# Kernel tuning notes

Hardware: AMD Instinct MI355X
Metric: run time of the kernel (lower is better)

## Reference

```python
import jax, jax.numpy as jnp
import numpy as np

L, N, C = 128, 32, 128
DIM_MLP, OUT = 128, 128


def setup_inputs() -> dict:
    key = jax.random.key(0)
    ks = jax.random.split(key, 6)
    s_in2 = 1.0 / np.sqrt(2 * C)
    s_mid = 1.0 / np.sqrt(DIM_MLP)
    s_in = 1.0 / np.sqrt(C)
    return {
        "x": jax.random.normal(ks[0], (L, N, C), jnp.float32),
        "attn_w1": jax.random.normal(ks[1], (2 * C, DIM_MLP), jnp.float32) * s_in2,
        "attn_b1": jnp.zeros((DIM_MLP,), jnp.float32),
        "attn_w2": jax.random.normal(ks[2], (DIM_MLP, OUT), jnp.float32) * s_mid,
        "attn_b2": jnp.zeros((OUT,), jnp.float32),
        "value_w1": jax.random.normal(ks[3], (C, DIM_MLP), jnp.float32) * s_in,
        "value_b1": jnp.zeros((DIM_MLP,), jnp.float32),
        "value_w2": jax.random.normal(ks[4], (DIM_MLP, OUT), jnp.float32) * s_mid,
        "value_b2": jnp.zeros((OUT,), jnp.float32),
    }


def reference(x, attn_w1, attn_b1, attn_w2, attn_b2,
              value_w1, value_b1, value_w2, value_b2):
    l, n, c = x.shape
    # Outer concat: pair[i, j, b] = concat(x[i, b], x[j, b])  -> (l, l, N, 2C)
    xi = jnp.broadcast_to(x[:, None, :, :], (l, l, n, c))
    xj = jnp.broadcast_to(x[None, :, :, :], (l, l, n, c))
    pair = jnp.concatenate([xi, xj], axis=-1)
    # Pairwise attention MLP (ReLU hidden, linear output)
    h = jax.nn.relu(pair @ attn_w1 + attn_b1)          # (l, l, N, dim_mlp)
    attn = h @ attn_w2 + attn_b2                       # (l, l, N, out)
    # Value MLP
    hv = jax.nn.relu(x @ value_w1 + value_b1)          # (l, N, dim_mlp)
    value = hv @ value_w2 + value_b2                   # (l, N, out)
    # Elementwise weighted reduce over key axis j (NOT a matmul over channels)
    out = jnp.einsum('ijbc,jbc->ibc', attn, value)     # (l, N, out)
    return out
```

## Files before the change

kernel.cpp:

```cpp
#include <hip/hip_runtime.h>
#include <hip/hip_bf16.h>

#define L_DIM 128
#define N_DIM 32
#define C_DIM 128
#define K_DIM 128
#define OUT_DIM 128

#define Q_STRIDE  132
#define VT_STRIDE 20

typedef __attribute__((ext_vector_type(8))) short short8;
typedef __attribute__((ext_vector_type(4))) float float4v;

static __device__ __forceinline__ short bf16_bits(float f) {
    __bf16 h = (__bf16)f;
    return __builtin_bit_cast(short, h);
}

__global__ __launch_bounds__(256) void k_pre(
    const float* __restrict__ x,
    const float* __restrict__ attn_w1, const float* __restrict__ attn_b1,
    const float* __restrict__ attn_w2,
    const float* __restrict__ value_w1, const float* __restrict__ value_b1,
    const float* __restrict__ value_w2, const float* __restrict__ value_b2,
    float* __restrict__ P, float* __restrict__ Q, float* __restrict__ Vt,
    short* __restrict__ W2s)
{
    int bid = blockIdx.x;
    if (bid >= 512) {
        int e = (bid - 512) * 256 + threadIdx.x;
        int idx  = e & 7;
        int colr = (e >> 3) & 15;
        int quad = (e >> 7) & 3;
        int mi   = (e >> 9) & 3;
        int ct   = e >> 11;
        int k = quad * 8 + 32 * mi + idx;
        int c = ct * 16 + colr;
        W2s[e] = bf16_bits(attn_w2[k * OUT_DIM + c]);
        return;
    }

    __shared__ float xs[8][C_DIM];
    __shared__ float hvs[8][K_DIM];
    int tid = threadIdx.x;
    int b   = bid >> 4;
    int i0g = (bid & 15) * 8;

    {
        int f = tid * 4;
        int row = f >> 7, c = f & 127;
        *(float4v*)(&xs[row][c]) =
            *(const float4v*)(x + ((size_t)(i0g + row) * N_DIM + b) * C_DIM + c);
    }
    __syncthreads();

    int ks   = tid & 127;
    int half = tid >> 7;

    float pacc[4] = {0,0,0,0};
    float qacc[4] = {0,0,0,0};
    float hacc[4] = {0,0,0,0};
    #pragma unroll 4
    for (int c = 0; c < C_DIM; ++c) {
        float wa = attn_w1[c * K_DIM + ks];
        float wb = attn_w1[(C_DIM + c) * K_DIM + ks];
        float wv = value_w1[c * K_DIM + ks];
        #pragma unroll
        for (int r = 0; r < 4; ++r) {
            float xr = xs[half * 4 + r][c];
            pacc[r] = fmaf(xr, wa, pacc[r]);
            qacc[r] = fmaf(xr, wb, qacc[r]);
            hacc[r] = fmaf(xr, wv, hacc[r]);
        }
    }
    float b1 = attn_b1[ks], vb1 = value_b1[ks];
    #pragma unroll
    for (int r = 0; r < 4; ++r) {
        int i = i0g + half * 4 + r;
        P[((size_t)b * L_DIM + i) * K_DIM + ks] = pacc[r];
        Q[((size_t)b * L_DIM + i) * K_DIM + ks] = qacc[r] + b1;
        hvs[half * 4 + r][ks] = fmaxf(hacc[r] + vb1, 0.f);
    }
    __syncthreads();

    float vacc[4] = {0,0,0,0};
    #pragma unroll 4
    for (int k = 0; k < K_DIM; ++k) {
        float w = value_w2[k * OUT_DIM + ks];
        #pragma unroll
        for (int r = 0; r < 4; ++r)
            vacc[r] = fmaf(hvs[half * 4 + r][k], w, vacc[r]);
    }
    float vb2 = value_b2[ks];
    float4v vout = { vacc[0] + vb2, vacc[1] + vb2, vacc[2] + vb2, vacc[3] + vb2 };
    *(float4v*)(Vt + ((size_t)b * OUT_DIM + ks) * L_DIM + i0g + half * 4) = vout;
}

__global__ __launch_bounds__(256, 2)
void k_main(
    const float* __restrict__ P, const float* __restrict__ Q,
    const float* __restrict__ Vt,
    const short* __restrict__ W2s, const float* __restrict__ attn_b2,
    float* __restrict__ out)
{
    __shared__ float Q_lds[2][16 * Q_STRIDE];
    __shared__ float Vt_lds[2][128 * VT_STRIDE];

    int b    = blockIdx.x >> 5;
    int it4  = blockIdx.x & 31;
    int tid  = threadIdx.x;
    int wave = tid >> 6;
    int lane = tid & 63;
    int quad = lane >> 4;
    int col  = lane & 15;
    int ip   = wave >> 1;
    int cth  = wave & 1;
    int i0   = it4 * 4 + ip * 2;

    short8 bfrag[4][4];
    const short8* w2p = (const short8*)W2s;
    #pragma unroll
    for (int cl = 0; cl < 4; ++cl)
        #pragma unroll
        for (int mi = 0; mi < 4; ++mi)
            bfrag[cl][mi] =
                w2p[(((cth * 4 + cl) * 4 + mi) * 4 + quad) * 16 + col];

    float4v pf[2][4][2];
    #pragma unroll
    for (int ii = 0; ii < 2; ++ii) {
        const float* Pp = P + ((size_t)b * L_DIM + i0 + ii) * K_DIM + quad * 8;
        #pragma unroll
        for (int ksl = 0; ksl < 4; ++ksl) {
            pf[ii][ksl][0] = *(const float4v*)(Pp + ksl * 32);
            pf[ii][ksl][1] = *(const float4v*)(Pp + ksl * 32 + 4);
        }
    }

    int srow = tid >> 4;
    int sc8  = (tid & 15) * 8;
    int cs   = tid >> 1;
    int ch   = (tid & 1) * 8;
    const float* Qbase = Q  + (size_t)b * L_DIM * K_DIM;
    const float* Vbase = Vt + (size_t)b * OUT_DIM * L_DIM;

    {
        const float* qp = Qbase + srow * K_DIM + sc8;
        float4v qa = *(const float4v*)qp, qb = *(const float4v*)(qp + 4);
        *(float4v*)&Q_lds[0][srow * Q_STRIDE + sc8]     = qa;
        *(float4v*)&Q_lds[0][srow * Q_STRIDE + sc8 + 4] = qb;
        const float* vp = Vbase + cs * L_DIM + ch;
        float4v va = *(const float4v*)vp, vb = *(const float4v*)(vp + 4);
        *(float4v*)&Vt_lds[0][cs * VT_STRIDE + ch]     = va;
        *(float4v*)&Vt_lds[0][cs * VT_STRIDE + ch + 4] = vb;
    }
    __syncthreads();

    float acc0[4] = {0.f, 0.f, 0.f, 0.f};
    float acc1[4] = {0.f, 0.f, 0.f, 0.f};
    float sv[4]   = {0.f, 0.f, 0.f, 0.f};

    for (int r = 0; r < 8; ++r) {
        int cur = r & 1;

        float4v nqa, nqb, nva, nvb;
        if (r < 7) {
            const float* qp = Qbase + ((r + 1) * 16 + srow) * K_DIM + sc8;
            nqa = *(const float4v*)qp; nqb = *(const float4v*)(qp + 4);
            const float* vp = Vbase + cs * L_DIM + (r + 1) * 16 + ch;
            nva = *(const float4v*)vp; nvb = *(const float4v*)(vp + 4);
        }

        short8 af[2][4];
        const float* Qc = &Q_lds[cur][col * Q_STRIDE + quad * 8];
        #pragma unroll
        for (int ksl = 0; ksl < 4; ++ksl) {
            float4v q0 = *(const float4v*)(Qc + ksl * 32);
            float4v q1 = *(const float4v*)(Qc + ksl * 32 + 4);
            #pragma unroll
            for (int ii = 0; ii < 2; ++ii) {
                float4v s0 = pf[ii][ksl][0] + q0;
                float4v s1 = pf[ii][ksl][1] + q1;
                short8 a;
                #pragma unroll
                for (int t = 0; t < 4; ++t) {
                    a[t]     = bf16_bits(fmaxf(s0[t], 0.f));
                    a[t + 4] = bf16_bits(fmaxf(s1[t], 0.f));
                }
                af[ii][ksl] = a;
            }
        }

        const float* Vc = &Vt_lds[cur][0];
        #pragma unroll
        for (int cl = 0; cl < 4; ++cl) {
            float4v c40 = {0.f, 0.f, 0.f, 0.f};
            float4v c41 = {0.f, 0.f, 0.f, 0.f};
            #pragma unroll
            for (int ksl = 0; ksl < 4; ++ksl) {
                c40 = __builtin_amdgcn_mfma_f32_16x16x32_bf16(
                        af[0][ksl], bfrag[cl][ksl], c40, 0, 0, 0);
                c41 = __builtin_amdgcn_mfma_f32_16x16x32_bf16(
                        af[1][ksl], bfrag[cl][ksl], c41, 0, 0, 0);
            }
            int cc = cth * 64 + cl * 16 + col;
            float4v vv = *(const float4v*)(Vc + cc * VT_STRIDE + quad * 4);
            #pragma unroll
            for (int rr = 0; rr < 4; ++rr) {
                acc0[cl] = fmaf(c40[rr], vv[rr], acc0[cl]);
                acc1[cl] = fmaf(c41[rr], vv[rr], acc1[cl]);
                sv[cl]  += vv[rr];
            }
        }

        if (r < 7) {
            int nxt = cur ^ 1;
            *(float4v*)&Q_lds[nxt][srow * Q_STRIDE + sc8]      = nqa;
            *(float4v*)&Q_lds[nxt][srow * Q_STRIDE + sc8 + 4]  = nqb;
            *(float4v*)&Vt_lds[nxt][cs * VT_STRIDE + ch]       = nva;
            *(float4v*)&Vt_lds[nxt][cs * VT_STRIDE + ch + 4]   = nvb;
            __syncthreads();
        }
    }

    #pragma unroll
    for (int cl = 0; cl < 4; ++cl) {
        acc0[cl] += __shfl_xor(acc0[cl], 16, 64);
        acc0[cl] += __shfl_xor(acc0[cl], 32, 64);
        acc1[cl] += __shfl_xor(acc1[cl], 16, 64);
        acc1[cl] += __shfl_xor(acc1[cl], 32, 64);
        sv[cl]   += __shfl_xor(sv[cl], 16, 64);
        sv[cl]   += __shfl_xor(sv[cl], 32, 64);
    }

    if (quad == 0) {
        #pragma unroll
        for (int cl = 0; cl < 4; ++cl) {
            int cc = cth * 64 + cl * 16 + col;
            float bsv = attn_b2[cc] * sv[cl];
            out[((size_t)i0 * N_DIM + b) * OUT_DIM + cc]       = acc0[cl] + bsv;
            out[((size_t)(i0 + 1) * N_DIM + b) * OUT_DIM + cc] = acc1[cl] + bsv;
        }
    }
}

extern "C" void kernel_launch(void* const* d_in, const int* in_sizes, int n_in,
                              void* d_out, int out_size, void* d_ws, size_t ws_size,
                              hipStream_t stream)
{
    const float* x        = (const float*)d_in[0];
    const float* attn_w1  = (const float*)d_in[1];
    const float* attn_b1  = (const float*)d_in[2];
    const float* attn_w2  = (const float*)d_in[3];
    const float* attn_b2  = (const float*)d_in[4];
    const float* value_w1 = (const float*)d_in[5];
    const float* value_b1 = (const float*)d_in[6];
    const float* value_w2 = (const float*)d_in[7];
    const float* value_b2 = (const float*)d_in[8];
    float* out = (float*)d_out;

    float* ws  = (float*)d_ws;
    float* P   = ws;
    float* Q   = ws + 524288;
    float* Vt  = ws + 1048576;
    short* W2s = (short*)(ws + 1572864);

    k_pre<<<576, 256, 0, stream>>>(x, attn_w1, attn_b1, attn_w2,
                                   value_w1, value_b1, value_w2, value_b2,
                                   P, Q, Vt, W2s);
    k_main<<<1024, 256, 0, stream>>>(P, Q, Vt, W2s, attn_b2, out);
}
```

Baseline: 126.1 us.

## Stage Q/V/P tiles via direct global-to-LDS loads with XOR swizzle

```diff
diff --git a/kernel.cpp b/kernel.cpp
--- a/kernel.cpp
+++ b/kernel.cpp
@@ -7,15 +7,18 @@
 #define K_DIM 128
 #define OUT_DIM 128
 
-#define Q_STRIDE  132
-#define VT_STRIDE 20
-
 typedef __attribute__((ext_vector_type(8))) short short8;
 typedef __attribute__((ext_vector_type(4))) float float4v;
 
 static __device__ __forceinline__ short bf16_bits(float f) {
     __bf16 h = (__bf16)f;
     return __builtin_bit_cast(short, h);
+}
+
+static __device__ __forceinline__ void gl_lds16(const float* g, float* l) {
+    __builtin_amdgcn_global_load_lds(
+        (const __attribute__((address_space(1))) unsigned int*)g,
+        (__attribute__((address_space(3))) unsigned int*)l, 16, 0, 0);
 }
 
 __global__ __launch_bounds__(256) void k_pre(
@@ -97,15 +100,17 @@
     *(float4v*)(Vt + ((size_t)b * OUT_DIM + ks) * L_DIM + i0g + half * 4) = vout;
 }
 
-__global__ __launch_bounds__(256, 2)
+__global__ __launch_bounds__(256)
+__attribute__((amdgpu_waves_per_eu(3)))
 void k_main(
     const float* __restrict__ P, const float* __restrict__ Q,
     const float* __restrict__ Vt,
     const short* __restrict__ W2s, const float* __restrict__ attn_b2,
     float* __restrict__ out)
 {
-    __shared__ float Q_lds[2][16 * Q_STRIDE];
-    __shared__ float Vt_lds[2][128 * VT_STRIDE];
+    __shared__ float Q_lds[2][16 * 128];
+    __shared__ float V_lds[2][128 * 16];
+    __shared__ float P_lds[4 * 128];
 
     int b    = blockIdx.x >> 5;
     int it4  = blockIdx.x & 31;
@@ -116,7 +121,9 @@
     int col  = lane & 15;
     int ip   = wave >> 1;
     int cth  = wave & 1;
-    int i0   = it4 * 4 + ip * 2;
+
+    const float* Qbase = Q  + (size_t)b * L_DIM * K_DIM;
+    const float* Vbase = Vt + (size_t)b * OUT_DIM * L_DIM;
 
     short8 bfrag[4][4];
     const short8* w2p = (const short8*)W2s;
@@ -127,61 +134,69 @@
             bfrag[cl][mi] =
                 w2p[(((cth * 4 + cl) * 4 + mi) * 4 + quad) * 16 + col];
 
-    float4v pf[2][4][2];
-    #pragma unroll
-    for (int ii = 0; ii < 2; ++ii) {
-        const float* Pp = P + ((size_t)b * L_DIM + i0 + ii) * K_DIM + quad * 8;
-        #pragma unroll
-        for (int ksl = 0; ksl < 4; ++ksl) {
-            pf[ii][ksl][0] = *(const float4v*)(Pp + ksl * 32);
-            pf[ii][ksl][1] = *(const float4v*)(Pp + ksl * 32 + 4);
-        }
-    }
-
-    int srow = tid >> 4;
-    int sc8  = (tid & 15) * 8;
-    int cs   = tid >> 1;
-    int ch   = (tid & 1) * 8;
-    const float* Qbase = Q  + (size_t)b * L_DIM * K_DIM;
-    const float* Vbase = Vt + (size_t)b * OUT_DIM * L_DIM;
-
-    {
-        const float* qp = Qbase + srow * K_DIM + sc8;
-        float4v qa = *(const float4v*)qp, qb = *(const float4v*)(qp + 4);
-        *(float4v*)&Q_lds[0][srow * Q_STRIDE + sc8]     = qa;
-        *(float4v*)&Q_lds[0][srow * Q_STRIDE + sc8 + 4] = qb;
-        const float* vp = Vbase + cs * L_DIM + ch;
-        float4v va = *(const float4v*)vp, vb = *(const float4v*)(vp + 4);
-        *(float4v*)&Vt_lds[0][cs * VT_STRIDE + ch]     = va;
-        *(float4v*)&Vt_lds[0][cs * VT_STRIDE + ch + 4] = vb;
+    int qinv[2], vinv[2];
+    #pragma unroll
+    for (int t = 0; t < 2; ++t) {
+        int n  = wave * 128 + t * 64 + lane;
+        int j  = n >> 5, c16 = n & 31;
+        int s8 = c16 >> 1, e = c16 & 1;
+        int g  = s8 ^ (j & 7);
+        qinv[t] = j * K_DIM + g * 8 + e * 4;
+        int c  = n >> 2, s = n & 3;
+        int ch = s ^ (c & 3);
+        vinv[t] = c * L_DIM + ch * 4;
+    }
+
+    #pragma unroll
+    for (int t = 0; t < 2; ++t) {
+        gl_lds16(Qbase + qinv[t], &Q_lds[0][wave * 512 + t * 256]);
+        gl_lds16(Vbase + vinv[t], &V_lds[0][wave * 512 + t * 256]);
+    }
+    if (wave == 0) {
+        #pragma unroll
+        for (int t = 0; t < 2; ++t) {
+            int n = t * 64 + lane;
+            gl_lds16(P + ((size_t)b * L_DIM + it4 * 4 + (n >> 5)) * K_DIM
+                       + (n & 31) * 4,
+                     &P_lds[t * 256]);
+        }
     }
     __syncthreads();
 
     float acc0[4] = {0.f, 0.f, 0.f, 0.f};
     float acc1[4] = {0.f, 0.f, 0.f, 0.f};
     float sv[4]   = {0.f, 0.f, 0.f, 0.f};
-
+    int pofs = 0;
+
+    #pragma unroll 1
     for (int r = 0; r < 8; ++r) {
         int cur = r & 1;
-
-        float4v nqa, nqb, nva, nvb;
+        asm volatile("" : "+v"(pofs));
+
         if (r < 7) {
-            const float* qp = Qbase + ((r + 1) * 16 + srow) * K_DIM + sc8;
-            nqa = *(const float4v*)qp; nqb = *(const float4v*)(qp + 4);
-            const float* vp = Vbase + cs * L_DIM + (r + 1) * 16 + ch;
-            nva = *(const float4v*)vp; nvb = *(const float4v*)(vp + 4);
+            int nxt = cur ^ 1;
+            #pragma unroll
+            for (int t = 0; t < 2; ++t) {
+                gl_lds16(Qbase + qinv[t] + (r + 1) * 16 * K_DIM,
+                         &Q_lds[nxt][wave * 512 + t * 256]);
+                gl_lds16(Vbase + vinv[t] + (r + 1) * 16,
+                         &V_lds[nxt][wave * 512 + t * 256]);
+            }
         }
 
         short8 af[2][4];
-        const float* Qc = &Q_lds[cur][col * Q_STRIDE + quad * 8];
+        const float* Qrow = &Q_lds[cur][col * 128];
+        const float* Prow = &P_lds[(ip * 2) * 128 + quad * 8 + pofs];
         #pragma unroll
         for (int ksl = 0; ksl < 4; ++ksl) {
-            float4v q0 = *(const float4v*)(Qc + ksl * 32);
-            float4v q1 = *(const float4v*)(Qc + ksl * 32 + 4);
+            int s8 = (ksl * 4 + quad) ^ (col & 7);
+            float4v q0 = *(const float4v*)(Qrow + s8 * 8);
+            float4v q1 = *(const float4v*)(Qrow + s8 * 8 + 4);
             #pragma unroll
             for (int ii = 0; ii < 2; ++ii) {
-                float4v s0 = pf[ii][ksl][0] + q0;
-                float4v s1 = pf[ii][ksl][1] + q1;
+                const float* Pc = Prow + ii * 128 + ksl * 32;
+                float4v s0 = *(const float4v*)Pc + q0;
+                float4v s1 = *(const float4v*)(Pc + 4) + q1;
                 short8 a;
                 #pragma unroll
                 for (int t = 0; t < 4; ++t) {
@@ -192,7 +207,6 @@
             }
         }
 
-        const float* Vc = &Vt_lds[cur][0];
         #pragma unroll
         for (int cl = 0; cl < 4; ++cl) {
             float4v c40 = {0.f, 0.f, 0.f, 0.f};
@@ -205,7 +219,8 @@
                         af[1][ksl], bfrag[cl][ksl], c41, 0, 0, 0);
             }
             int cc = cth * 64 + cl * 16 + col;
-            float4v vv = *(const float4v*)(Vc + cc * VT_STRIDE + quad * 4);
+            float4v vv = *(const float4v*)
+                (&V_lds[cur][cc * 16 + ((quad ^ (cc & 3)) << 2)]);
             #pragma unroll
             for (int rr = 0; rr < 4; ++rr) {
                 acc0[cl] = fmaf(c40[rr], vv[rr], acc0[cl]);
@@ -214,14 +229,7 @@
             }
         }
 
-        if (r < 7) {
-            int nxt = cur ^ 1;
-            *(float4v*)&Q_lds[nxt][srow * Q_STRIDE + sc8]      = nqa;
-            *(float4v*)&Q_lds[nxt][srow * Q_STRIDE + sc8 + 4]  = nqb;
-            *(float4v*)&Vt_lds[nxt][cs * VT_STRIDE + ch]       = nva;
-            *(float4v*)&Vt_lds[nxt][cs * VT_STRIDE + ch + 4]   = nvb;
-            __syncthreads();
-        }
+        if (r < 7) __syncthreads();
     }
 
     #pragma unroll
@@ -235,6 +243,7 @@
     }
 
     if (quad == 0) {
+        int i0 = it4 * 4 + ip * 2;
         #pragma unroll
         for (int cl = 0; cl < 4; ++cl) {
             int cc = cth * 64 + cl * 16 + col;
```

After: 124.6 us. About the same (-1.2%).
